# Optimization experiments

Measured on AMD Instinct MI355X. Metric: run time of the kernel, lower is better.

Reference implementation:

```python
import jax, jax.numpy as jnp
import numpy as np

N_NODES = 50000
N_EDGES = 800000
NFEAT, NHID, NCLASS = 128, 256, 64


def setup_inputs() -> dict:
    key = jax.random.key(0)
    ks = jax.random.split(key, 8)
    x = jax.random.normal(ks[0], (N_NODES, NFEAT), dtype=jnp.float32)
    edge_index = jax.random.randint(ks[1], (2, N_EDGES), 0, N_NODES, dtype=jnp.int64)
    s1 = 1.0 / np.sqrt(NFEAT)
    s2 = 1.0 / np.sqrt(NHID)
    W1_neigh = jax.random.normal(ks[2], (NFEAT, NHID), dtype=jnp.float32) * s1
    W1_root = jax.random.normal(ks[3], (NFEAT, NHID), dtype=jnp.float32) * s1
    b1 = jnp.zeros((NHID,), dtype=jnp.float32)
    W2_neigh = jax.random.normal(ks[4], (NHID, NCLASS), dtype=jnp.float32) * s2
    W2_root = jax.random.normal(ks[5], (NHID, NCLASS), dtype=jnp.float32) * s2
    b2 = jnp.zeros((NCLASS,), dtype=jnp.float32)
    return {"x": x, "edge_index": edge_index, "W1_neigh": W1_neigh,
            "W1_root": W1_root, "b1": b1, "W2_neigh": W2_neigh,
            "W2_root": W2_root, "b2": b2}


def _sage_conv(h, src, dst, n_nodes, W_neigh, W_root, b):
    # mean aggregation of source features into destination nodes
    msg = h[src]                                                   # [E, d]
    summed = jax.ops.segment_sum(msg, dst, num_segments=n_nodes)   # [N, d]
    cnt = jax.ops.segment_sum(jnp.ones((src.shape[0],), h.dtype), dst,
                              num_segments=n_nodes)                # [N]
    mean = summed / jnp.maximum(cnt, 1.0)[:, None]
    return mean @ W_neigh + h @ W_root + b


def reference(x, edge_index, W1_neigh, W1_root, b1, W2_neigh, W2_root, b2):
    src, dst = edge_index[0], edge_index[1]
    n = x.shape[0]
    h = jax.nn.relu(_sage_conv(x, src, dst, n, W1_neigh, W1_root, b1))
    # dropout is identity in eval mode
    out = _sage_conv(h, src, dst, n, W2_neigh, W2_root, b2)
    return out
```

## Files before the change

### kernel.cpp

```cpp
#include <hip/hip_runtime.h>

#define N_NODES 50000
#define N_EDGES 800000
#define NFEAT   128
#define NHID    256
#define NCLASS  64

#define ELLCAP  64

#define NBUCK   56
#define BWIDTH  896
#define BCAP    16384
#define BIN_CH  4096
#define BIN_B   ((N_EDGES + BIN_CH - 1) / BIN_CH)
#define NFINE   ((N_NODES + 127) / 128)
#define NFINE2  ((N_NODES + 63) / 64)
#define FPB     7

#define CVTX_B  ((N_NODES * 32 + 255) / 256)
#define CVTW_B  (((65536 + 32768) + 255) / 256)

typedef unsigned short u16;
typedef unsigned int   u32;
typedef __attribute__((ext_vector_type(8))) short s16x8;
typedef __attribute__((ext_vector_type(4))) float f32x4;

__device__ inline u16 f2bf(float f) {
    u32 u = __float_as_uint(f);
    u32 r = (u + 0x7FFFu + ((u >> 16) & 1u)) >> 16;
    return (u16)r;
}
__device__ inline float bflo(u32 v) { return __uint_as_float(v << 16); }
__device__ inline float bfhi(u32 v) { return __uint_as_float(v & 0xFFFF0000u); }

#define GLOAD_LDS16(g, l)                                                        \
    __builtin_amdgcn_global_load_lds(                                            \
        (const __attribute__((address_space(1))) u32*)(const void*)(g),          \
        (__attribute__((address_space(3))) u32*)(void*)(l), 16, 0, 0)

__global__ __launch_bounds__(256) void prep_kernel(const float* __restrict__ x,
                                                   const int* __restrict__ ei,
                                                   const float* __restrict__ W1r,
                                                   const float* __restrict__ W1n,
                                                   const float* __restrict__ W2n,
                                                   const float* __restrict__ W2r,
                                                   u16* __restrict__ xa,
                                                   u32* __restrict__ gcnt,
                                                   u32* __restrict__ bbuf,
                                                   u16* __restrict__ W1t,
                                                   u16* __restrict__ W2t) {
    int b = blockIdx.x;
    if (b < BIN_B) {
        __shared__ u32 hist[NBUCK];
        __shared__ u32 base[NBUCK];
        int tid = threadIdx.x;
        if (tid < NBUCK) hist[tid] = 0;
        __syncthreads();
        u32 ek[16]; u32 rk[16]; int bk[16];
        int i0 = b * BIN_CH;
        #pragma unroll
        for (int k = 0; k < 16; ++k) {
            int i = i0 + k * 256 + tid;
            bk[k] = -1;
            if (i < N_EDGES) {
                u32 s = (u32)ei[i];
                u32 d = (u32)ei[N_EDGES + i];
                int bu = (int)(d / BWIDTH);
                ek[k] = (d << 16) | s;
                bk[k] = bu;
                rk[k] = atomicAdd(&hist[bu], 1u);
            }
        }
        __syncthreads();
        if (tid < NBUCK) base[tid] = atomicAdd(&gcnt[tid], hist[tid]);
        __syncthreads();
        #pragma unroll
        for (int k = 0; k < 16; ++k) {
            if (bk[k] >= 0) {
                u32 pos = base[bk[k]] + rk[k];
                if (pos < BCAP) bbuf[((u32)bk[k] << 14) + pos] = ek[k];
            }
        }
    } else if (b < BIN_B + CVTX_B) {
        int idx = (b - BIN_B) * 256 + threadIdx.x;
        if (idx >= N_NODES * 32) return;
        int r  = idx >> 5;
        int c4 = (idx & 31) * 4;
        float4 v = *reinterpret_cast<const float4*>(x + (size_t)r * NFEAT + c4);
        uint2 o;
        o.x = (u32)f2bf(v.x) | ((u32)f2bf(v.y) << 16);
        o.y = (u32)f2bf(v.z) | ((u32)f2bf(v.w) << 16);
        *reinterpret_cast<uint2*>(xa + (size_t)r * 256 + c4) = o;
    } else {
        int id = (b - BIN_B - CVTX_B) * 256 + threadIdx.x;
        if (id < 65536) {
            int k = id & 255, n = id >> 8;
            float v = (k < NFEAT) ? W1r[(size_t)k * NHID + n]
                                  : W1n[(size_t)(k - NFEAT) * NHID + n];
            W1t[(size_t)n * 256 + k] = f2bf(v);
        } else if (id < 65536 + 32768) {
            int j = id - 65536;
            int k = j & 255, n = j >> 8;
            float v = (n < NCLASS) ? W2n[(size_t)k * NCLASS + n]
                                   : W2r[(size_t)k * NCLASS + (n - NCLASS)];
            W2t[(size_t)n * 256 + k] = f2bf(v);
        }
    }
}

__global__ __launch_bounds__(512) void ell_build_kernel(const u32* __restrict__ bbuf,
                                                        const u32* __restrict__ gcnt,
                                                        int* __restrict__ cnt,
                                                        u16* __restrict__ ell) {
    __shared__ u32 hist[128];
    int tid = threadIdx.x;
    int f   = blockIdx.x;
    int cb  = f / FPB;
    int n0  = f * 128;
    if (tid < 128) hist[tid] = 0;
    __syncthreads();
    int m = (int)gcnt[cb]; if (m > BCAP) m = BCAP;
    const u32* bk = bbuf + ((u32)cb << 14);
    int i = tid;
    for (; i + 1536 < m; i += 2048) {
        u32 e0 = bk[i], e1 = bk[i + 512], e2 = bk[i + 1024], e3 = bk[i + 1536];
        u32 d0 = (e0 >> 16) - (u32)n0, d1 = (e1 >> 16) - (u32)n0;
        u32 d2 = (e2 >> 16) - (u32)n0, d3 = (e3 >> 16) - (u32)n0;
        if (d0 < 128u) { u32 p = atomicAdd(&hist[d0], 1u); if (p < ELLCAP) ell[(size_t)(n0 + (int)d0) * ELLCAP + p] = (u16)e0; }
        if (d1 < 128u) { u32 p = atomicAdd(&hist[d1], 1u); if (p < ELLCAP) ell[(size_t)(n0 + (int)d1) * ELLCAP + p] = (u16)e1; }
        if (d2 < 128u) { u32 p = atomicAdd(&hist[d2], 1u); if (p < ELLCAP) ell[(size_t)(n0 + (int)d2) * ELLCAP + p] = (u16)e2; }
        if (d3 < 128u) { u32 p = atomicAdd(&hist[d3], 1u); if (p < ELLCAP) ell[(size_t)(n0 + (int)d3) * ELLCAP + p] = (u16)e3; }
    }
    for (; i < m; i += 512) {
        u32 e = bk[i];
        u32 d = (e >> 16) - (u32)n0;
        if (d < 128u) { u32 p = atomicAdd(&hist[d], 1u); if (p < ELLCAP) ell[(size_t)(n0 + (int)d) * ELLCAP + p] = (u16)e; }
    }
    __syncthreads();
    if (tid < 128) cnt[n0 + tid] = (int)hist[tid];
}

#define ACC8(v)                                                      \
    do { a[0] += bflo((v).x); a[1] += bfhi((v).x);                   \
         a[2] += bflo((v).y); a[3] += bfhi((v).y);                   \
         a[4] += bflo((v).z); a[5] += bfhi((v).z);                   \
         a[6] += bflo((v).w); a[7] += bfhi((v).w); } while (0)

__global__ __launch_bounds__(256) void gather1_kernel(const int* __restrict__ cnt,
                                                      const u16* __restrict__ ell,
                                                      u16* __restrict__ xa) {
    int gtid = blockIdx.x * 256 + threadIdx.x;
    int node = gtid >> 6;
    if (node >= N_NODES) return;
    int lane = threadIdx.x & 63;
    int g = lane >> 4, lr = lane & 15;
    const u32* xrow = reinterpret_cast<const u32*>(xa);
    const u16* idx = ell + (size_t)node * ELLCAP;
    int deg = cnt[node];
    if (deg > ELLCAP) deg = ELLCAP;
    float a[8] = {};
    int j = 0;
    for (; j + 16 <= deg; j += 16) {
        int s0 = idx[j + g], s1 = idx[j + 4 + g], s2 = idx[j + 8 + g], s3 = idx[j + 12 + g];
        uint4 v0 = *reinterpret_cast<const uint4*>(xrow + (size_t)s0 * 128 + lr * 4);
        uint4 v1 = *reinterpret_cast<const uint4*>(xrow + (size_t)s1 * 128 + lr * 4);
        uint4 v2 = *reinterpret_cast<const uint4*>(xrow + (size_t)s2 * 128 + lr * 4);
        uint4 v3 = *reinterpret_cast<const uint4*>(xrow + (size_t)s3 * 128 + lr * 4);
        ACC8(v0); ACC8(v1); ACC8(v2); ACC8(v3);
    }
    for (; j + 4 <= deg; j += 4) {
        int s0 = idx[j + g];
        uint4 v0 = *reinterpret_cast<const uint4*>(xrow + (size_t)s0 * 128 + lr * 4);
        ACC8(v0);
    }
    if (g < deg - j) {
        int s0 = idx[j + g];
        uint4 v0 = *reinterpret_cast<const uint4*>(xrow + (size_t)s0 * 128 + lr * 4);
        ACC8(v0);
    }
    #pragma unroll
    for (int k = 0; k < 8; ++k) {
        a[k] += __shfl_xor(a[k], 16);
        a[k] += __shfl_xor(a[k], 32);
    }
    if (g == 0) {
        float invd = 1.0f / fmaxf((float)deg, 1.0f);
        uint4 pk;
        pk.x = (u32)f2bf(a[0] * invd) | ((u32)f2bf(a[1] * invd) << 16);
        pk.y = (u32)f2bf(a[2] * invd) | ((u32)f2bf(a[3] * invd) << 16);
        pk.z = (u32)f2bf(a[4] * invd) | ((u32)f2bf(a[5] * invd) << 16);
        pk.w = (u32)f2bf(a[6] * invd) | ((u32)f2bf(a[7] * invd) << 16);
        *reinterpret_cast<uint4*>(reinterpret_cast<u32*>(xa) + (size_t)node * 128 + 64 + lr * 4) = pk;
    }
}

__global__ __launch_bounds__(256) void gather2_kernel(const int* __restrict__ cnt,
                                                      const u16* __restrict__ ell,
                                                      const u16* __restrict__ t,
                                                      float* __restrict__ out) {
    int gtid = blockIdx.x * 256 + threadIdx.x;
    int node = gtid >> 6;
    if (node >= N_NODES) return;
    int lane = threadIdx.x & 63;
    int g = lane >> 3, lr = lane & 7;
    const u32* trow = reinterpret_cast<const u32*>(t);
    const u16* idx = ell + (size_t)node * ELLCAP;
    int deg = cnt[node];
    if (deg > ELLCAP) deg = ELLCAP;
    float a[8] = {};
    int j = 0;
    for (; j + 16 <= deg; j += 16) {
        int s0 = idx[j + g], s1 = idx[j + 8 + g];
        uint4 v0 = *reinterpret_cast<const uint4*>(trow + (size_t)s0 * 32 + lr * 4);
        uint4 v1 = *reinterpret_cast<const uint4*>(trow + (size_t)s1 * 32 + lr * 4);
        ACC8(v0); ACC8(v1);
    }
    for (; j + 8 <= deg; j += 8) {
        int s0 = idx[j + g];
        uint4 v0 = *reinterpret_cast<const uint4*>(trow + (size_t)s0 * 32 + lr * 4);
        ACC8(v0);
    }
    if (g < deg - j) {
        int s0 = idx[j + g];
        uint4 v0 = *reinterpret_cast<const uint4*>(trow + (size_t)s0 * 32 + lr * 4);
        ACC8(v0);
    }
    #pragma unroll
    for (int k = 0; k < 8; ++k) {
        a[k] += __shfl_xor(a[k], 8);
        a[k] += __shfl_xor(a[k], 16);
        a[k] += __shfl_xor(a[k], 32);
    }
    if (g == 0) {
        float invd = 1.0f / fmaxf((float)deg, 1.0f);
        float* o = out + (size_t)node * NCLASS + lr * 8;
        float4 o0 = *reinterpret_cast<float4*>(o);
        float4 o1 = *reinterpret_cast<float4*>(o + 4);
        o0.x += a[0] * invd; o0.y += a[1] * invd; o0.z += a[2] * invd; o0.w += a[3] * invd;
        o1.x += a[4] * invd; o1.y += a[5] * invd; o1.z += a[6] * invd; o1.w += a[7] * invd;
        *reinterpret_cast<float4*>(o) = o0;
        *reinterpret_cast<float4*>(o + 4) = o1;
    }
}

__global__ __launch_bounds__(256) void gemm12_fused(const u16* __restrict__ xa,
                                                    const u16* __restrict__ W1t,
                                                    const float* __restrict__ b1,
                                                    const u16* __restrict__ W2t,
                                                    const float* __restrict__ b2,
                                                    u16* __restrict__ t,
                                                    float* __restrict__ out) {
    __shared__ u16 Af[64 * 256];
    __shared__ u16 Bs[2][128 * 32];
    __shared__ u16 hs[64 * 256];
    const int tid = threadIdx.x;
    const int r0 = blockIdx.x * 64;
    const int wid = tid >> 6, ln = tid & 63;
    const int wm = (wid & 1) * 32, wn = (wid >> 1) * 64;
    const int lr = ln & 15;
    const int lq = ln >> 4;

    #pragma unroll
    for (int p = 0; p < 8; ++p) {
        int c    = p * 256 + tid;
        int row  = c >> 5;
        int col8 = (c & 31) ^ (row & 7);
        GLOAD_LDS16(xa + (size_t)(r0 + row) * 256 + col8 * 8, Af + c * 8);
    }
    #pragma unroll
    for (int it = 0; it < 2; ++it) {
        int c = it * 256 + tid;
        GLOAD_LDS16(W1t + (size_t)(c >> 2) * 256 + (c & 3) * 8, &Bs[0][0] + c * 8);
    }
    __syncthreads();

    f32x4 acc[2][4] = {};
    int cur = 0;
    #pragma unroll 1
    for (int s = 0; s < 24; ++s) {
        if (s < 23) {
            int sn = s + 1;
            const u16* bsrc = (sn < 8) ? W1t : (sn < 16) ? (W1t + 128 * 256) : W2t;
            int k0n = (sn & 7) * 32;
            #pragma unroll
            for (int it = 0; it < 2; ++it) {
                int c = it * 256 + tid;
                GLOAD_LDS16(bsrc + (size_t)(c >> 2) * 256 + k0n + (c & 3) * 8,
                            &Bs[cur ^ 1][0] + c * 8);
            }
        }

        int k0 = (s & 7) * 32;
        const u16* asrc = (s < 16) ? Af : hs;
        s16x8 af[2], bf[4];
        #pragma unroll
        for (int i = 0; i < 2; ++i) {
            int row = wm + i * 16 + lr;
            af[i] = *reinterpret_cast<const s16x8*>(
                asrc + row * 256 + ((k0 + lq * 8) ^ ((row & 7) << 3)));
        }
        #pragma unroll
        for (int j = 0; j < 4; ++j)
            bf[j] = *reinterpret_cast<const s16x8*>(&Bs[cur][0] + (wn + j * 16 + lr) * 32 + lq * 8);
        #pragma unroll
        for (int i = 0; i < 2; ++i)
            #pragma unroll
            for (int j = 0; j < 4; ++j)
                acc[i][j] = __builtin_amdgcn_mfma_f32_16x16x32_bf16(af[i], bf[j], acc[i][j], 0, 0, 0);

        if (s == 7 || s == 15) {
            int half = s >> 3;
            #pragma unroll
            for (int i = 0; i < 2; ++i) {
                #pragma unroll
                for (int j = 0; j < 4; ++j) {
                    int col = half * 128 + wn + j * 16 + lr;
                    float bias = b1[col];
                    #pragma unroll
                    for (int r = 0; r < 4; ++r) {
                        int row = wm + i * 16 + lq * 4 + r;
                        hs[row * 256 + (col ^ ((row & 7) << 3))] =
                            f2bf(fmaxf(acc[i][j][r] + bias, 0.0f));
                        acc[i][j][r] = 0.0f;
                    }
                }
            }
        }
        __syncthreads();
        cur ^= 1;
    }

    #pragma unroll
    for (int i = 0; i < 2; ++i) {
        #pragma unroll
        for (int j = 0; j < 4; ++j) {
            int col = wn + j * 16 + lr;
            #pragma unroll
            for (int r = 0; r < 4; ++r) {
                int row = r0 + wm + i * 16 + lq * 4 + r;
                if (row >= N_NODES) continue;
                if (col < NCLASS) {
                    t[(size_t)row * NCLASS + col] = f2bf(acc[i][j][r]);
                } else {
                    int c = col - NCLASS;
                    out[(size_t)row * NCLASS + c] = acc[i][j][r] + b2[c];
                }
            }
        }
    }
}

extern "C" void kernel_launch(void* const* d_in, const int* in_sizes, int n_in,
                              void* d_out, int out_size, void* d_ws, size_t ws_size,
                              hipStream_t stream) {
    const float* x    = (const float*)d_in[0];
    const int*   ei   = (const int*)d_in[1];
    const float* W1n  = (const float*)d_in[2];
    const float* W1r  = (const float*)d_in[3];
    const float* b1   = (const float*)d_in[4];
    const float* W2n  = (const float*)d_in[5];
    const float* W2r  = (const float*)d_in[6];
    const float* b2   = (const float*)d_in[7];
    float* out = (float*)d_out;

    u32* gcnt = (u32*)d_ws;
    u32* bbuf = gcnt + 64;
    int* cnt  = (int*)(bbuf + ((size_t)NBUCK << 14));
    u16* ell  = (u16*)(cnt + 50048);
    u16* xa   = ell + (size_t)N_NODES * ELLCAP;
    u16* t    = xa + (size_t)50048 * 256;
    u16* W1t  = t  + (size_t)N_NODES * 64;
    u16* W2t  = W1t + 65536;

    hipMemsetAsync(gcnt, 0, 64 * sizeof(u32), stream);

    prep_kernel<<<BIN_B + CVTX_B + CVTW_B, 256, 0, stream>>>(
        x, ei, W1r, W1n, W2n, W2r, xa, gcnt, bbuf, W1t, W2t);
    ell_build_kernel<<<NFINE, 512, 0, stream>>>(bbuf, gcnt, cnt, ell);

    gather1_kernel<<<(N_NODES * 64 + 255) / 256, 256, 0, stream>>>(cnt, ell, xa);

    gemm12_fused<<<NFINE2, 256, 0, stream>>>(xa, W1t, b1, W2t, b2, t, out);

    gather2_kernel<<<(N_NODES * 64 + 255) / 256, 256, 0, stream>>>(cnt, ell, t, out);
}
```

Measured before the change: 206.0 us.

## Keep layer-1 A tile in registers instead of LDS in fused GEMM

The 64x256 input tile is now loaded straight from global memory into per-wave registers rather than staged in shared memory. This frees 32KB of LDS per block, and a launch bound of 3 blocks per SM is added so occupancy can rise. The 24-step loop is restructured into 3 phases of 8 fully unrolled steps, so register-resident A fragments can be indexed statically. The trade-off is more register pressure (64 VGPRs for A), which together with the occupancy cap could cause spills.

```diff
diff --git a/kernel.cpp b/kernel.cpp
--- a/kernel.cpp
+++ b/kernel.cpp
@@ -243,14 +243,13 @@
     }
 }
 
-__global__ __launch_bounds__(256) void gemm12_fused(const u16* __restrict__ xa,
-                                                    const u16* __restrict__ W1t,
-                                                    const float* __restrict__ b1,
-                                                    const u16* __restrict__ W2t,
-                                                    const float* __restrict__ b2,
-                                                    u16* __restrict__ t,
-                                                    float* __restrict__ out) {
-    __shared__ u16 Af[64 * 256];
+__global__ __launch_bounds__(256, 3) void gemm12_fused(const u16* __restrict__ xa,
+                                                       const u16* __restrict__ W1t,
+                                                       const float* __restrict__ b1,
+                                                       const u16* __restrict__ W2t,
+                                                       const float* __restrict__ b2,
+                                                       u16* __restrict__ t,
+                                                       float* __restrict__ out) {
     __shared__ u16 Bs[2][128 * 32];
     __shared__ u16 hs[64 * 256];
     const int tid = threadIdx.x;
@@ -260,74 +259,85 @@
     const int lr = ln & 15;
     const int lq = ln >> 4;
 
+    {
+        int c0 = tid, c1 = 256 + tid;
+        GLOAD_LDS16(W1t + (size_t)(c0 >> 2) * 256 + (c0 & 3) * 8, &Bs[0][0] + c0 * 8);
+        GLOAD_LDS16(W1t + (size_t)(c1 >> 2) * 256 + (c1 & 3) * 8, &Bs[0][0] + c1 * 8);
+    }
+    s16x8 areg[2][8];
     #pragma unroll
-    for (int p = 0; p < 8; ++p) {
-        int c    = p * 256 + tid;
-        int row  = c >> 5;
-        int col8 = (c & 31) ^ (row & 7);
-        GLOAD_LDS16(xa + (size_t)(r0 + row) * 256 + col8 * 8, Af + c * 8);
-    }
-    #pragma unroll
-    for (int it = 0; it < 2; ++it) {
-        int c = it * 256 + tid;
-        GLOAD_LDS16(W1t + (size_t)(c >> 2) * 256 + (c & 3) * 8, &Bs[0][0] + c * 8);
-    }
+    for (int i = 0; i < 2; ++i)
+        #pragma unroll
+        for (int k = 0; k < 8; ++k)
+            areg[i][k] = *reinterpret_cast<const s16x8*>(
+                xa + (size_t)(r0 + wm + i * 16 + lr) * 256 + k * 32 + lq * 8);
     __syncthreads();
 
     f32x4 acc[2][4] = {};
-    int cur = 0;
     #pragma unroll 1
-    for (int s = 0; s < 24; ++s) {
-        if (s < 23) {
-            int sn = s + 1;
-            const u16* bsrc = (sn < 8) ? W1t : (sn < 16) ? (W1t + 128 * 256) : W2t;
-            int k0n = (sn & 7) * 32;
-            #pragma unroll
-            for (int it = 0; it < 2; ++it) {
-                int c = it * 256 + tid;
-                GLOAD_LDS16(bsrc + (size_t)(c >> 2) * 256 + k0n + (c & 3) * 8,
-                            &Bs[cur ^ 1][0] + c * 8);
-            }
-        }
-
-        int k0 = (s & 7) * 32;
-        const u16* asrc = (s < 16) ? Af : hs;
-        s16x8 af[2], bf[4];
-        #pragma unroll
-        for (int i = 0; i < 2; ++i) {
-            int row = wm + i * 16 + lr;
-            af[i] = *reinterpret_cast<const s16x8*>(
-                asrc + row * 256 + ((k0 + lq * 8) ^ ((row & 7) << 3)));
-        }
-        #pragma unroll
-        for (int j = 0; j < 4; ++j)
-            bf[j] = *reinterpret_cast<const s16x8*>(&Bs[cur][0] + (wn + j * 16 + lr) * 32 + lq * 8);
-        #pragma unroll
-        for (int i = 0; i < 2; ++i)
+    for (int ph = 0; ph < 3; ++ph) {
+        #pragma unroll
+        for (int k = 0; k < 8; ++k) {
+            int s = ph * 8 + k;
+            if (s < 23) {
+                const u16* bsrc = (s + 1 < 8) ? W1t
+                                 : (s + 1 < 16) ? (W1t + 128 * 256) : W2t;
+                int k0n = ((k + 1) & 7) * 32;
+                int c0 = tid, c1 = 256 + tid;
+                GLOAD_LDS16(bsrc + (size_t)(c0 >> 2) * 256 + k0n + (c0 & 3) * 8,
+                            &Bs[(k & 1) ^ 1][0] + c0 * 8);
+                GLOAD_LDS16(bsrc + (size_t)(c1 >> 2) * 256 + k0n + (c1 & 3) * 8,
+                            &Bs[(k & 1) ^ 1][0] + c1 * 8);
+            }
+
+            s16x8 bf[4];
             #pragma unroll
             for (int j = 0; j < 4; ++j)
-                acc[i][j] = __builtin_amdgcn_mfma_f32_16x16x32_bf16(af[i], bf[j], acc[i][j], 0, 0, 0);
-
-        if (s == 7 || s == 15) {
-            int half = s >> 3;
-            #pragma unroll
-            for (int i = 0; i < 2; ++i) {
+                bf[j] = *reinterpret_cast<const s16x8*>(
+                    &Bs[k & 1][0] + (wn + j * 16 + lr) * 32 + lq * 8);
+
+            if (ph < 2) {
                 #pragma unroll
-                for (int j = 0; j < 4; ++j) {
-                    int col = half * 128 + wn + j * 16 + lr;
-                    float bias = b1[col];
+                for (int i = 0; i < 2; ++i)
                     #pragma unroll
-                    for (int r = 0; r < 4; ++r) {
-                        int row = wm + i * 16 + lq * 4 + r;
-                        hs[row * 256 + (col ^ ((row & 7) << 3))] =
-                            f2bf(fmaxf(acc[i][j][r] + bias, 0.0f));
-                        acc[i][j][r] = 0.0f;
+                    for (int j = 0; j < 4; ++j)
+                        acc[i][j] = __builtin_amdgcn_mfma_f32_16x16x32_bf16(
+                            areg[i][k], bf[j], acc[i][j], 0, 0, 0);
+            } else {
+                s16x8 af[2];
+                #pragma unroll
+                for (int i = 0; i < 2; ++i) {
+                    int row = wm + i * 16 + lr;
+                    af[i] = *reinterpret_cast<const s16x8*>(
+                        hs + row * 256 + ((k * 32 + lq * 8) ^ ((row & 7) << 3)));
+                }
+                #pragma unroll
+                for (int i = 0; i < 2; ++i)
+                    #pragma unroll
+                    for (int j = 0; j < 4; ++j)
+                        acc[i][j] = __builtin_amdgcn_mfma_f32_16x16x32_bf16(
+                            af[i], bf[j], acc[i][j], 0, 0, 0);
+            }
+
+            if (k == 7 && ph < 2) {
+                #pragma unroll
+                for (int i = 0; i < 2; ++i) {
+                    #pragma unroll
+                    for (int j = 0; j < 4; ++j) {
+                        int col = ph * 128 + wn + j * 16 + lr;
+                        float bias = b1[col];
+                        #pragma unroll
+                        for (int r = 0; r < 4; ++r) {
+                            int row = wm + i * 16 + lq * 4 + r;
+                            hs[row * 256 + (col ^ ((row & 7) << 3))] =
+                                f2bf(fmaxf(acc[i][j][r] + bias, 0.0f));
+                            acc[i][j][r] = 0.0f;
+                        }
                     }
                 }
             }
-        }
-        __syncthreads();
-        cur ^= 1;
+            __syncthreads();
+        }
     }
 
     #pragma unroll
```

After: 218.1 us. 1.06x slower.
